# Optimization experiments

Measured on AMD Instinct MI355X. Metric: run time of the kernel, lower is better.

## Reference

```python
import jax, jax.numpy as jnp
import numpy as np

B, HG, WG = 2, 64, 64
N = HG * WG
C_IN, C_HID, HEADS, C_OUT = 512, 256, 4, 512
NEG_SLOPE = 0.2   # PyG GATv2Conv default negative_slope
LN_EPS = 1e-5


def _grid_edges(h, w):
    """8-neighborhood grid graph, edge_index[0]=source, edge_index[1]=target."""
    nodes = np.arange(h * w).reshape(h, w)
    srcs, dsts = [], []
    for dh in (-1, 0, 1):
        for dw in (-1, 0, 1):
            if dh == 0 and dw == 0:
                continue
            r0, r1 = max(0, -dh), h - max(0, dh)
            c0, c1 = max(0, -dw), w - max(0, dw)
            srcs.append(nodes[r0:r1, c0:c1].ravel())
            dsts.append(nodes[r0 + dh:r1 + dh, c0 + dw:c1 + dw].ravel())
    return np.stack([np.concatenate(srcs), np.concatenate(dsts)]).astype(np.int64)


def setup_inputs() -> dict:
    key = jax.random.key(0)
    ks = iter(jax.random.split(key, 32))

    def p(shape, scale=0.02):
        return jax.random.normal(next(ks), shape, dtype=jnp.float32) * scale

    return {
        "rgb_features": jax.random.normal(next(ks), (B, N, C_IN), dtype=jnp.float32),
        "x_features": jax.random.normal(next(ks), (B, N, C_IN), dtype=jnp.float32),
        "edge_index": jnp.asarray(_grid_edges(HG, WG)),
        # modality_fusion: Linear(2*C_IN, C_HID) + LayerNorm
        "fusion_w": p((C_HID, 2 * C_IN)), "fusion_b": jnp.zeros((C_HID,), jnp.float32),
        "fusion_g": jnp.ones((C_HID,), jnp.float32), "fusion_beta": jnp.zeros((C_HID,), jnp.float32),
        # GATSegmentation.in_proj + norm
        "inproj_w": p((C_HID, C_HID)), "inproj_b": jnp.zeros((C_HID,), jnp.float32),
        "norm_g": jnp.ones((C_HID,), jnp.float32), "norm_b": jnp.zeros((C_HID,), jnp.float32),
        # GATv2Conv layer 0: C_HID -> C_HID, heads=4, concat=True
        "l0_wl": p((HEADS * C_HID, C_HID)), "l0_bl": jnp.zeros((HEADS * C_HID,), jnp.float32),
        "l0_wr": p((HEADS * C_HID, C_HID)), "l0_br": jnp.zeros((HEADS * C_HID,), jnp.float32),
        "l0_att": p((HEADS, C_HID)), "l0_bias": jnp.zeros((HEADS * C_HID,), jnp.float32),
        # GATv2Conv layer 1 (final): 4*C_HID -> C_HID, heads=1, concat=False
        "l1_wl": p((C_HID, HEADS * C_HID)), "l1_bl": jnp.zeros((C_HID,), jnp.float32),
        "l1_wr": p((C_HID, HEADS * C_HID)), "l1_br": jnp.zeros((C_HID,), jnp.float32),
        "l1_att": p((1, C_HID)), "l1_bias": jnp.zeros((C_HID,), jnp.float32),
        # final_proj: 1x1 conv C_HID -> C_OUT
        "fp_w": p((C_OUT, C_HID)), "fp_b": jnp.zeros((C_OUT,), jnp.float32),
    }


def _ln(x, g, b):
    mu = x.mean(-1, keepdims=True)
    v = ((x - mu) ** 2).mean(-1, keepdims=True)
    return (x - mu) * jax.lax.rsqrt(v + LN_EPS) * g + b


def _gatv2(x, src, dst, wl, bl, wr, br, att, bias, concat):
    """PyG GATv2Conv (share_weights=False): gather, leaky_relu logit, segment softmax over
    target neighborhoods, scatter-add aggregation."""
    n = x.shape[0]
    heads, c = att.shape
    xl = (x @ wl.T + bl).reshape(n, heads, c)   # source-side transform (x_j)
    xr = (x @ wr.T + br).reshape(n, heads, c)   # target-side transform (x_i)
    e = jax.nn.leaky_relu(xl[src] + xr[dst], NEG_SLOPE)        # [E, H, C]
    logit = jnp.einsum('ehc,hc->eh', e, att)                   # [E, H]
    m = jax.ops.segment_max(logit, dst, num_segments=n)
    p = jnp.exp(logit - m[dst])
    z = jax.ops.segment_sum(p, dst, num_segments=n)
    alpha = p / z[dst]                                          # softmax per target node
    out = jax.ops.segment_sum(xl[src] * alpha[..., None], dst, num_segments=n)  # [N, H, C]
    out = out.reshape(n, heads * c) if concat else out.mean(axis=1)
    return out + bias


def reference(rgb_features, x_features, edge_index, fusion_w, fusion_b, fusion_g, fusion_beta,
              inproj_w, inproj_b, norm_g, norm_b,
              l0_wl, l0_bl, l0_wr, l0_br, l0_att, l0_bias,
              l1_wl, l1_bl, l1_wr, l1_br, l1_att, l1_bias,
              fp_w, fp_b):
    b, n, _ = rgb_features.shape
    loops = jnp.arange(n, dtype=edge_index.dtype)  # PyG add_self_loops=True
    src = jnp.concatenate([edge_index[0], loops])
    dst = jnp.concatenate([edge_index[1], loops])

    def single(rgb, xm):  # one graph in the batch (original loops over B in Python)
        comb = jnp.concatenate([rgb, xm], axis=-1)                     # [N, 2*C_IN]
        f = jax.nn.relu(_ln(comb @ fusion_w.T + fusion_b, fusion_g, fusion_beta))
        h = jax.nn.relu(_ln(f @ inproj_w.T + inproj_b, norm_g, norm_b))
        h = jax.nn.relu(_gatv2(h, src, dst, l0_wl, l0_bl, l0_wr, l0_br, l0_att, l0_bias, True))
        h = jax.nn.relu(_gatv2(h, src, dst, l1_wl, l1_bl, l1_wr, l1_br, l1_att, l1_bias, False))
        return h                                                        # [N, C_HID]

    nodes = jax.vmap(single)(rgb_features, x_features)                  # [B, N, C_HID]
    img = nodes.reshape(b, HG, WG, C_HID)
    return jnp.einsum('bhwc,oc->bohw', img, fp_w) + fp_b[None, :, None, None]
```

## Files before the change

### kernel.cpp

```cpp
#include <hip/hip_runtime.h>


#define NNODE 4096
#define LN_EPS 1e-5f
#define LOG2E 1.4426950408889634f

typedef _Float16 half8 __attribute__((ext_vector_type(8)));
typedef _Float16 half4 __attribute__((ext_vector_type(4)));
typedef _Float16 h2 __attribute__((ext_vector_type(2)));
typedef float f32x4 __attribute__((ext_vector_type(4)));

__device__ __forceinline__ float wave_reduce_sum(float v) {
    #pragma unroll
    for (int off = 32; off > 0; off >>= 1) v += __shfl_xor(v, off, 64);
    return v;
}

__device__ __forceinline__ void gload_lds16(const void* g, void* l) {
    __builtin_amdgcn_global_load_lds(
        (const __attribute__((address_space(1))) void*)g,
        (__attribute__((address_space(3))) void*)l, 16, 0, 0);
}

template<int N> __device__ __forceinline__ void waitcnt_vm() {
    if constexpr (N <= 0)      asm volatile("s_waitcnt vmcnt(0)" ::: "memory");
    else if constexpr (N == 2) asm volatile("s_waitcnt vmcnt(2)" ::: "memory");
    else if constexpr (N == 3) asm volatile("s_waitcnt vmcnt(3)" ::: "memory");
    else if constexpr (N == 4) asm volatile("s_waitcnt vmcnt(4)" ::: "memory");
    else                       asm volatile("s_waitcnt vmcnt(8)" ::: "memory");
}
__device__ __forceinline__ void lgkm0() {
    asm volatile("s_waitcnt lgkmcnt(0)" ::: "memory");
}
__device__ __forceinline__ void barrier_raw() {
    asm volatile("s_barrier" ::: "memory");
}

template<int IT, int JT, int OUTMODE>
__global__ __launch_bounds__(256) void gemm3_k(
    const _Float16* __restrict__ A, const _Float16* __restrict__ W,
    const float* __restrict__ bias_lo, const float* __restrict__ bias_hi,
    int nsplit, void* __restrict__ Cout, int K, int N)
{
    constexpr int BM = 32 * IT, BN = 32 * JT;
    constexpr int CA = (BM * 4) / 256;
    constexpr int CB = (BN * 4) / 256;
    constexpr int L = CA + CB;
    __shared__ _Float16 ldsA[3][BM * 32];
    __shared__ _Float16 ldsB[3][BN * 32];

    const int tid = threadIdx.x;
    const int m0 = blockIdx.y * BM, n0 = blockIdx.x * BN;
    const int lane = tid & 63, w = tid >> 6;
    const int fr = lane & 15, kq = lane >> 4;
    const int sq = (kq ^ (fr & 3)) * 8;
    const int wm = (w & 1) * (16 * IT), wn = (w >> 1) * (16 * JT);

    const _Float16* aP[CA]; int aC[CA];
    #pragma unroll
    for (int i = 0; i < CA; ++i) {
        const int c = i * 256 + tid, r = c >> 2, q = (c & 3) ^ (r & 3);
        aP[i] = A + (size_t)(m0 + r) * K + q * 8;
        aC[i] = c * 8;
    }
    const _Float16* bP[CB]; int bC[CB];
    #pragma unroll
    for (int i = 0; i < CB; ++i) {
        const int c = i * 256 + tid, r = c >> 2, q = (c & 3) ^ (r & 3);
        bP[i] = W + (size_t)(n0 + r) * K + q * 8;
        bC[i] = c * 8;
    }

    f32x4 acc[IT][JT] = {};
    const int NT = K >> 5;

    #pragma unroll
    for (int i = 0; i < CA; ++i) gload_lds16(aP[i], &ldsA[0][aC[i]]);
    #pragma unroll
    for (int i = 0; i < CB; ++i) gload_lds16(bP[i], &ldsB[0][bC[i]]);
    #pragma unroll
    for (int i = 0; i < CA; ++i) gload_lds16(aP[i] + 32, &ldsA[1][aC[i]]);
    #pragma unroll
    for (int i = 0; i < CB; ++i) gload_lds16(bP[i] + 32, &ldsB[1][bC[i]]);

    int bi = 0;
    for (int t = 0; t < NT; ++t) {
        if (t + 1 < NT) waitcnt_vm<L>(); else waitcnt_vm<0>();
        barrier_raw();
        if (t + 2 < NT) {
            int nb = bi + 2; if (nb >= 3) nb -= 3;
            const int k2 = (t + 2) << 5;
            #pragma unroll
            for (int i = 0; i < CA; ++i) gload_lds16(aP[i] + k2, &ldsA[nb][aC[i]]);
            #pragma unroll
            for (int i = 0; i < CB; ++i) gload_lds16(bP[i] + k2, &ldsB[nb][bC[i]]);
        }
        half8 af[IT], bf[JT];
        #pragma unroll
        for (int i = 0; i < IT; ++i)
            af[i] = *(const half8*)&ldsA[bi][(wm + i * 16 + fr) * 32 + sq];
        #pragma unroll
        for (int j = 0; j < JT; ++j)
            bf[j] = *(const half8*)&ldsB[bi][(wn + j * 16 + fr) * 32 + sq];
        #pragma unroll
        for (int i = 0; i < IT; ++i)
            #pragma unroll
            for (int j = 0; j < JT; ++j)
                acc[i][j] = __builtin_amdgcn_mfma_f32_16x16x32_f16(
                    bf[j], af[i], acc[i][j], 0, 0, 0);
        ++bi; if (bi == 3) bi = 0;
    }

    #pragma unroll
    for (int i = 0; i < IT; ++i) {
        const int m = m0 + wm + i * 16 + fr;
        #pragma unroll
        for (int j = 0; j < JT; ++j) {
            const int nb4 = n0 + wn + j * 16 + kq * 4;
            const float* bp = (nb4 < nsplit) ? bias_lo + nb4
                                             : bias_hi + (nb4 - nsplit);
            const float4 bv = *(const float4*)bp;
            half4 ov = {(_Float16)(acc[i][j][0] + bv.x),
                        (_Float16)(acc[i][j][1] + bv.y),
                        (_Float16)(acc[i][j][2] + bv.z),
                        (_Float16)(acc[i][j][3] + bv.w)};
            *(half4*)((_Float16*)Cout + (size_t)m * N + nb4) = ov;
        }
    }
}

struct ConvTab {
    const float* src[7];
    int startblk[8];
    int nelem[7];
    int dstoff[7];
    float scale[7];
};

__global__ __launch_bounds__(512) void fusion2b_k(
    const float* __restrict__ A0, const float* __restrict__ A1,
    const float* __restrict__ W1f, const float* __restrict__ b1,
    const float* __restrict__ g1, const float* __restrict__ be1,
    const float* __restrict__ W2f, const float* __restrict__ b2,
    const float* __restrict__ g2, const float* __restrict__ be2,
    _Float16* __restrict__ out, _Float16* __restrict__ wdst, ConvTab ct)
{
    if (blockIdx.x >= 256) {
        const int cid = blockIdx.x - 256;
        int s = 0;
        #pragma unroll
        for (int i = 1; i < 7; ++i) s += (cid >= ct.startblk[i]);
        const int e0 = (cid - ct.startblk[s]) * 2048 + threadIdx.x * 4;
        if (e0 < ct.nelem[s]) {
            const float4 v = *(const float4*)(ct.src[s] + e0);
            const float sc = ct.scale[s];
            half4 o = {(_Float16)(v.x * sc), (_Float16)(v.y * sc),
                       (_Float16)(v.z * sc), (_Float16)(v.w * sc)};
            *(half4*)(wdst + ct.dstoff[s] + e0) = o;
        }
        return;
    }

    __shared__ _Float16 lA[2][32 * 32];
    __shared__ _Float16 lB[2][256 * 32];
    __shared__ float lC[32 * 260];
    __shared__ _Float16 lH[8 * 1024];

    const int tid = threadIdx.x;
    const int m0 = blockIdx.x * 32;
    const int lane = tid & 63, w = tid >> 6;
    const int fr = lane & 15, kq = lane >> 4;
    const int sq = (kq ^ (fr & 3)) * 8;
    const int wr = (w & 1) * 16, wc = (w >> 1) * 64;
    const bool stager = (tid < 128);

    const int br_ = tid >> 3, bf_ = tid & 7;
    const int bq_ = bf_ >> 1, bo_ = bf_ & 1;
    float4 pb[4];

    const int ar = tid >> 2, aq = tid & 3;
    const int asw = (ar * 4 + (aq ^ (ar & 3))) * 8;
    float4 pa0, pa1;

    auto loadB = [&](const float* Wf, int ldw, int k0) {
        #pragma unroll
        for (int i = 0; i < 4; ++i)
            pb[i] = *(const float4*)(Wf + (size_t)(br_ + i * 64) * ldw + k0 + bf_ * 4);
    };
    auto writeB = [&](int buf) {
        #pragma unroll
        for (int i = 0; i < 4; ++i) {
            const int r = br_ + i * 64;
            half4 o = {(_Float16)pb[i].x, (_Float16)pb[i].y,
                       (_Float16)pb[i].z, (_Float16)pb[i].w};
            *(half4*)&lB[buf][(r * 4 + (bq_ ^ (r & 3))) * 8 + bo_ * 4] = o;
        }
    };
    auto loadA = [&](int k) {
        const int gk = k + aq * 8;
        const float* s = (gk < 512) ? A0 + (size_t)(m0 + ar) * 512 + gk
                                    : A1 + (size_t)(m0 + ar) * 512 + gk - 512;
        pa0 = *(const float4*)s;
        pa1 = *(const float4*)(s + 4);
    };
    auto writeA = [&](int buf) {
        half8 hv = {(_Float16)pa0.x, (_Float16)pa0.y, (_Float16)pa0.z, (_Float16)pa0.w,
                    (_Float16)pa1.x, (_Float16)pa1.y, (_Float16)pa1.z, (_Float16)pa1.w};
        *(half8*)&lA[buf][asw] = hv;
    };

    f32x4 acc1[4] = {};
    if (stager) { loadA(0); writeA(0); loadA(32); }
    loadB(W1f, 1024, 0); writeB(0); loadB(W1f, 1024, 32);
    lgkm0(); barrier_raw();
    for (int t = 0; t < 32; ++t) {
        if (t + 1 < 32) { writeB((t + 1) & 1); if (stager) writeA((t + 1) & 1); }
        lgkm0(); barrier_raw();
        if (t + 2 < 32) { loadB(W1f, 1024, (t + 2) * 32); if (stager) loadA((t + 2) * 32); }
        const half8 af = *(const half8*)&lA[t & 1][(wr + fr) * 32 + sq];
        half8 bfr[4];
        #pragma unroll
        for (int j = 0; j < 4; ++j)
            bfr[j] = *(const half8*)&lB[t & 1][(wc + j * 16 + fr) * 32 + sq];
        #pragma unroll
        for (int j = 0; j < 4; ++j)
            acc1[j] = __builtin_amdgcn_mfma_f32_16x16x32_f16(af, bfr[j], acc1[j], 0, 0, 0);
        lgkm0(); barrier_raw();
    }

    #pragma unroll
    for (int j = 0; j < 4; ++j) {
        const int col = wc + j * 16 + fr;
        const float bc = b1[col];
        #pragma unroll
        for (int r4 = 0; r4 < 4; ++r4)
            lC[(wr + kq * 4 + r4) * 260 + col] = acc1[j][r4] + bc;
    }
    __syncthreads();

    {
        const float4 gv = *(const float4*)(g1 + lane * 4);
        const float4 bv = *(const float4*)(be1 + lane * 4);
        const int t2i = lane >> 3, gq = (lane >> 1) & 3, qo = (lane & 1) * 4;
        #pragma unroll
        for (int rr = 0; rr < 4; ++rr) {
            const int row = w * 4 + rr;
            const float4 v = *(const float4*)&lC[row * 260 + lane * 4];
            float s  = v.x + v.y + v.z + v.w;
            float s2 = v.x * v.x + v.y * v.y + v.z * v.z + v.w * v.w;
            s = wave_reduce_sum(s);
            s2 = wave_reduce_sum(s2);
            const float mu  = s * (1.0f / 256.0f);
            const float var = s2 * (1.0f / 256.0f) - mu * mu;
            const float rs  = rsqrtf(var + LN_EPS);
            half4 o;
            o[0] = (_Float16)fmaxf((v.x - mu) * rs * gv.x + bv.x, 0.f);
            o[1] = (_Float16)fmaxf((v.y - mu) * rs * gv.y + bv.y, 0.f);
            o[2] = (_Float16)fmaxf((v.z - mu) * rs * gv.z + bv.z, 0.f);
            o[3] = (_Float16)fmaxf((v.w - mu) * rs * gv.w + bv.w, 0.f);
            const int qslot = gq ^ (row & 3);
            *(half4*)&lH[t2i * 1024 + (row * 4 + qslot) * 8 + qo] = o;
        }
    }
    __syncthreads();

    f32x4 acc2[4] = {};
    loadB(W2f, 256, 0); writeB(0); loadB(W2f, 256, 32);
    lgkm0(); barrier_raw();
    for (int t = 0; t < 8; ++t) {
        if (t + 1 < 8) writeB((t + 1) & 1);
        lgkm0(); barrier_raw();
        if (t + 2 < 8) loadB(W2f, 256, (t + 2) * 32);
        const half8 af = *(const half8*)
            &lH[t * 1024 + ((wr + fr) * 4 + (kq ^ (fr & 3))) * 8];
        half8 bfr[4];
        #pragma unroll
        for (int j = 0; j < 4; ++j)
            bfr[j] = *(const half8*)&lB[t & 1][(wc + j * 16 + fr) * 32 + sq];
        #pragma unroll
        for (int j = 0; j < 4; ++j)
            acc2[j] = __builtin_amdgcn_mfma_f32_16x16x32_f16(af, bfr[j], acc2[j], 0, 0, 0);
        lgkm0(); barrier_raw();
    }

    #pragma unroll
    for (int j = 0; j < 4; ++j) {
        const int col = wc + j * 16 + fr;
        const float bc = b2[col];
        #pragma unroll
        for (int r4 = 0; r4 < 4; ++r4)
            lC[(wr + kq * 4 + r4) * 260 + col] = acc2[j][r4] + bc;
    }
    __syncthreads();

    {
        const float4 gv = *(const float4*)(g2 + lane * 4);
        const float4 bv = *(const float4*)(be2 + lane * 4);
        #pragma unroll
        for (int rr = 0; rr < 4; ++rr) {
            const int row = w * 4 + rr;
            const float4 v = *(const float4*)&lC[row * 260 + lane * 4];
            float s  = v.x + v.y + v.z + v.w;
            float s2 = v.x * v.x + v.y * v.y + v.z * v.z + v.w * v.w;
            s = wave_reduce_sum(s);
            s2 = wave_reduce_sum(s2);
            const float mu  = s * (1.0f / 256.0f);
            const float var = s2 * (1.0f / 256.0f) - mu * mu;
            const float rs  = rsqrtf(var + LN_EPS);
            half4 o;
            o[0] = (_Float16)fmaxf((v.x - mu) * rs * gv.x + bv.x, 0.f);
            o[1] = (_Float16)fmaxf((v.y - mu) * rs * gv.y + bv.y, 0.f);
            o[2] = (_Float16)fmaxf((v.z - mu) * rs * gv.z + bv.z, 0.f);
            o[3] = (_Float16)fmaxf((v.w - mu) * rs * gv.w + bv.w, 0.f);
            *(half4*)(out + (size_t)(m0 + row) * 256 + lane * 4) = o;
        }
    }
}

template<int HEADS, int K, int LD, int XROFF, int OUTMODE>
__global__ __launch_bounds__(512) void gatgemm_k(
    const _Float16* __restrict__ xlr, const _Float16* __restrict__ att16,
    const float* __restrict__ gbias, const _Float16* __restrict__ W,
    const float* __restrict__ bias_lo, const float* __restrict__ bias_hi,
    int nsplit, void* __restrict__ Cout)
{
    constexpr int PAD = K + 8;
    constexpr int NT = K / 32;
    __shared__ _Float16 lA[32 * PAD];
    __shared__ _Float16 lB[2][512 * 32];

    const int tid = threadIdx.x;
    const int m0 = blockIdx.x * 32;
    const int lane = tid & 63, w = tid >> 6;
    const int g = lane >> 4, li = lane & 15;

    const _Float16* bP[4]; int bC[4];
    #pragma unroll
    for (int i = 0; i < 4; ++i) {
        const int c = i * 512 + tid, r = c >> 2, q = (c & 3) ^ (r & 3);
        bP[i] = W + (size_t)r * K + q * 8;
        bC[i] = c * 8;
    }
    #pragma unroll
    for (int i = 0; i < 4; ++i) gload_lds16(bP[i], &lB[0][bC[i]]);
    #pragma unroll
    for (int i = 0; i < 4; ++i) gload_lds16(bP[i] + 32, &lB[1][bC[i]]);

    const int rounds = (HEADS == 4) ? 4 : 1;
    for (int rr = 0; rr < rounds; ++rr) {
        const int row = (HEADS == 4) ? (w * 4 + rr) : (w * 4 + g);
        const int gi = m0 + row;
        const int node = gi & (NNODE - 1);
        const int base = gi - node;
        const int h = (HEADS == 4) ? g : 0;
        const int nr = node >> 6, nc = node & 63;
        const int co = h * 256 + li * 16;

        int sidx[9]; float msk[9];
        {
            const int drs[8] = {-1,-1,-1, 0, 0, 1, 1, 1};
            const int dcs[8] = {-1, 0, 1,-1, 1,-1, 0, 1};
            #pragma unroll
            for (int j = 0; j < 8; ++j) {
                const int rj = nr + drs[j], cj = nc + dcs[j];
                const bool v = ((unsigned)rj < 64u) & ((unsigned)cj < 64u);
                sidx[j] = v ? (rj * 64 + cj) : node;
                msk[j] = v ? 0.f : -1e30f;
            }
            sidx[8] = node; msk[8] = 0.f;
        }
        const _Float16* xp = xlr + (size_t)base * LD + co;
        const half8 xr0 = *(const half8*)(xlr + (size_t)gi * LD + XROFF + co);
        const half8 xr1 = *(const half8*)(xlr + (size_t)gi * LD + XROFF + co + 8);
        const half8 at0 = *(const half8*)(att16 + h * 256 + li * 16);
        const half8 at1 = *(const half8*)(att16 + h * 256 + li * 16 + 8);
        const h2 hz = {(_Float16)0.f, (_Float16)0.f};
        const h2 c02 = {(_Float16)0.2f, (_Float16)0.2f};

        float lg[9];
        #pragma unroll
        for (int j = 0; j < 9; ++j) {
            const half8 x0 = *(const half8*)(xp + (size_t)sidx[j] * LD);
            const half8 x1 = *(const half8*)(xp + (size_t)sidx[j] * LD + 8);
            h2 p = hz;
            #pragma unroll
            for (int k = 0; k < 4; ++k) {
                h2 e = ((const h2*)&x0)[k] + ((const h2*)&xr0)[k];
                h2 tt = __builtin_elementwise_fma(
                    __builtin_elementwise_min(e, hz), c02,
                    __builtin_elementwise_max(e, hz));
                p = __builtin_elementwise_fma(tt, ((const h2*)&at0)[k], p);
            }
            #pragma unroll
            for (int k = 0; k < 4; ++k) {
                h2 e = ((const h2*)&x1)[k] + ((const h2*)&xr1)[k];
                h2 tt = __builtin_elementwise_fma(
                    __builtin_elementwise_min(e, hz), c02,
                    __builtin_elementwise_max(e, hz));
                p = __builtin_elementwise_fma(tt, ((const h2*)&at1)[k], p);
            }
            float pl = (float)p[0] + (float)p[1];
            pl += __shfl_xor(pl, 1, 64);
            pl += __shfl_xor(pl, 2, 64);
            pl += __shfl_xor(pl, 4, 64);
            pl += __shfl_xor(pl, 8, 64);
            lg[j] = pl + msk[j];
        }
        float m = lg[0];
        #pragma unroll
        for (int j = 1; j < 9; ++j) m = fmaxf(m, lg[j]);
        float pj[9], z = 0.f;
        #pragma unroll
        for (int j = 0; j < 9; ++j) { pj[j] = __builtin_amdgcn_exp2f(lg[j] - m); z += pj[j]; }
        const float inv = __builtin_amdgcn_rcpf(z);

        float acc[16];
        #pragma unroll
        for (int k = 0; k < 16; ++k) acc[k] = 0.f;
        #pragma unroll
        for (int j = 0; j < 9; ++j) {
            const half8 x0 = *(const half8*)(xp + (size_t)sidx[j] * LD);
            const half8 x1 = *(const half8*)(xp + (size_t)sidx[j] * LD + 8);
            const float wj = pj[j];
            #pragma unroll
            for (int k = 0; k < 8; ++k) acc[k]     += wj * (float)x0[k];
            #pragma unroll
            for (int k = 0; k < 8; ++k) acc[8 + k] += wj * (float)x1[k];
        }
        float bv[16];
        #pragma unroll
        for (int q = 0; q < 4; ++q) {
            const float4 b4 = *(const float4*)(gbias + h * 256 + li * 16 + q * 4);
            bv[q * 4 + 0] = b4.x; bv[q * 4 + 1] = b4.y;
            bv[q * 4 + 2] = b4.z; bv[q * 4 + 3] = b4.w;
        }
        half8 o0, o1;
        #pragma unroll
        for (int k = 0; k < 8; ++k) o0[k] = (_Float16)fmaxf(acc[k] * inv + bv[k], 0.f);
        #pragma unroll
        for (int k = 0; k < 8; ++k) o1[k] = (_Float16)fmaxf(acc[8 + k] * inv + bv[8 + k], 0.f);
        *(half8*)&lA[row * PAD + co] = o0;
        *(half8*)&lA[row * PAD + co + 8] = o1;
    }
    __syncthreads();

    const int fr = lane & 15, kq = lane >> 4;
    const int sq = (kq ^ (fr & 3)) * 8;
    const int wc = w * 64;
    f32x4 acc[2][4] = {};

    for (int t = 0; t < NT; ++t) {
        if (t + 1 < NT) waitcnt_vm<4>(); else waitcnt_vm<0>();
        barrier_raw();
        half8 af[2]; half8 bfr[4];
        #pragma unroll
        for (int i = 0; i < 2; ++i)
            af[i] = *(const half8*)&lA[(i * 16 + fr) * PAD + t * 32 + kq * 8];
        #pragma unroll
        for (int j = 0; j < 4; ++j)
            bfr[j] = *(const half8*)&lB[t & 1][(wc + j * 16 + fr) * 32 + sq];
        lgkm0(); barrier_raw();
        if (t + 2 < NT) {
            #pragma unroll
            for (int i = 0; i < 4; ++i)
                gload_lds16(bP[i] + (t + 2) * 32, &lB[t & 1][bC[i]]);
        }
        #pragma unroll
        for (int i = 0; i < 2; ++i)
            #pragma unroll
            for (int j = 0; j < 4; ++j) {
                if (OUTMODE == 1)
                    acc[i][j] = __builtin_amdgcn_mfma_f32_16x16x32_f16(
                        bfr[j], af[i], acc[i][j], 0, 0, 0);
                else
                    acc[i][j] = __builtin_amdgcn_mfma_f32_16x16x32_f16(
                        af[i], bfr[j], acc[i][j], 0, 0, 0);
            }
    }

    if (OUTMODE == 1) {
        #pragma unroll
        for (int i = 0; i < 2; ++i) {
            const int m = m0 + i * 16 + fr;
            #pragma unroll
            for (int j = 0; j < 4; ++j) {
                const int nb4 = wc + j * 16 + kq * 4;
                const float* bp = (nb4 < nsplit) ? bias_lo + nb4
                                                 : bias_hi + (nb4 - nsplit);
                const float4 bvv = *(const float4*)bp;
                half4 ov = {(_Float16)(acc[i][j][0] + bvv.x),
                            (_Float16)(acc[i][j][1] + bvv.y),
                            (_Float16)(acc[i][j][2] + bvv.z),
                            (_Float16)(acc[i][j][3] + bvv.w)};
                *(half4*)((_Float16*)Cout + (size_t)m * 512 + nb4) = ov;
            }
        }
    } else {
        #pragma unroll
        for (int j = 0; j < 4; ++j) {
            const int col = wc + j * 16 + fr;
            const float bc = bias_lo[col];
            #pragma unroll
            for (int i = 0; i < 2; ++i) {
                const int mrun = m0 + i * 16 + kq * 4;
                const int b = mrun >> 12, node = mrun & 4095;
                float4 ov = {acc[i][j][0] + bc, acc[i][j][1] + bc,
                             acc[i][j][2] + bc, acc[i][j][3] + bc};
                *(float4*)((float*)Cout + ((size_t)(b * 512 + col)) * 4096 + node) = ov;
            }
        }
    }
}

extern "C" void kernel_launch(void* const* d_in, const int* in_sizes, int n_in,
                              void* d_out, int out_size, void* d_ws, size_t ws_size,
                              hipStream_t stream)
{
    const float* rgb       = (const float*)d_in[0];
    const float* xm        = (const float*)d_in[1];
    const float* fusion_w  = (const float*)d_in[3];
    const float* fusion_b  = (const float*)d_in[4];
    const float* fusion_g  = (const float*)d_in[5];
    const float* fusion_be = (const float*)d_in[6];
    const float* inproj_w  = (const float*)d_in[7];
    const float* inproj_b  = (const float*)d_in[8];
    const float* norm_g    = (const float*)d_in[9];
    const float* norm_b    = (const float*)d_in[10];
    const float* l0_wl     = (const float*)d_in[11];
    const float* l0_bl     = (const float*)d_in[12];
    const float* l0_wr     = (const float*)d_in[13];
    const float* l0_br     = (const float*)d_in[14];
    const float* l0_att    = (const float*)d_in[15];
    const float* l0_bias   = (const float*)d_in[16];
    const float* l1_wl     = (const float*)d_in[17];
    const float* l1_bl     = (const float*)d_in[18];
    const float* l1_wr     = (const float*)d_in[19];
    const float* l1_br     = (const float*)d_in[20];
    const float* l1_att    = (const float*)d_in[21];
    const float* l1_bias   = (const float*)d_in[22];
    const float* fp_w      = (const float*)d_in[23];
    const float* fp_b      = (const float*)d_in[24];

    char* ws = (char*)d_ws;
    _Float16* Wf16 = (_Float16*)ws;
    _Float16* H1   = (_Float16*)(ws + 4194304);
    _Float16* XLR0 = (_Float16*)(ws + 8388608);
    _Float16* XLR1 = (_Float16*)(ws + 41943040);

    _Float16* w_l0   = Wf16 + 327680;
    _Float16* w_l1   = Wf16 + 851968;
    _Float16* w_fp   = Wf16 + 1376256;
    _Float16* att0_h = Wf16 + 1507328;
    _Float16* att1_h = Wf16 + 1508352;

    ConvTab ct;
    const float* srcs[7] = {l0_wl, l0_wr, l1_wl, l1_wr, fp_w, l0_att, l1_att};
    const int nel[7]  = {262144, 262144, 262144, 262144, 131072, 1024, 256};
    const int doff[7] = {327680, 589824, 851968, 1114112, 1376256, 1507328, 1508352};
    const int sblk[8] = {0, 128, 256, 384, 512, 576, 577, 578};
    for (int i = 0; i < 7; ++i) {
        ct.src[i] = srcs[i]; ct.nelem[i] = nel[i]; ct.dstoff[i] = doff[i];
        ct.scale[i] = (i >= 5) ? LOG2E : 1.0f;
    }
    for (int i = 0; i < 8; ++i) ct.startblk[i] = sblk[i];

    fusion2b_k<<<834, 512, 0, stream>>>(
        rgb, xm, fusion_w, fusion_b, fusion_g, fusion_be,
        inproj_w, inproj_b, norm_g, norm_b, H1, Wf16, ct);

    gemm3_k<4, 4, 1><<<dim3(16, 64), 256, 0, stream>>>(
        H1, w_l0, l0_bl, l0_br, 1024, XLR0, 256, 2048);

    gatgemm_k<4, 1024, 2048, 1024, 1><<<256, 512, 0, stream>>>(
        XLR0, att0_h, l0_bias, w_l1, l1_bl, l1_br, 256, XLR1);

    gatgemm_k<1, 256, 512, 256, 2><<<256, 512, 0, stream>>>(
        XLR1, att1_h, l1_bias, w_fp, fp_b, fp_b, 512, d_out);
}
```

Measured before the change: 127.3 us.

## Split fused GAT+GEMM kernels into standalone attention and GEMM launches

Replaces the fused attention-plus-GEMM kernel, which ran only 256 blocks of 512 threads with heavy LDS use, with a separate wave-per-node attention kernel that writes an fp16 intermediate, followed by the general pipelined GEMM kernel. The GEMM kernel gains a transposed-output mode so it can write the final NCHW float output. The aim is better occupancy and a more efficient GEMM pipeline. The cost is two extra launches and a round trip of the attention outputs through global memory. The attention kernel also preloads all nine neighbour vectors into registers instead of loading them twice.

```diff
diff --git a/kernel.cpp b/kernel.cpp
--- a/kernel.cpp
+++ b/kernel.cpp
@@ -105,26 +105,47 @@
         #pragma unroll
         for (int i = 0; i < IT; ++i)
             #pragma unroll
-            for (int j = 0; j < JT; ++j)
-                acc[i][j] = __builtin_amdgcn_mfma_f32_16x16x32_f16(
-                    bf[j], af[i], acc[i][j], 0, 0, 0);
+            for (int j = 0; j < JT; ++j) {
+                if (OUTMODE == 1)
+                    acc[i][j] = __builtin_amdgcn_mfma_f32_16x16x32_f16(
+                        bf[j], af[i], acc[i][j], 0, 0, 0);
+                else
+                    acc[i][j] = __builtin_amdgcn_mfma_f32_16x16x32_f16(
+                        af[i], bf[j], acc[i][j], 0, 0, 0);
+            }
         ++bi; if (bi == 3) bi = 0;
     }
 
-    #pragma unroll
-    for (int i = 0; i < IT; ++i) {
-        const int m = m0 + wm + i * 16 + fr;
+    if (OUTMODE == 1) {
+        #pragma unroll
+        for (int i = 0; i < IT; ++i) {
+            const int m = m0 + wm + i * 16 + fr;
+            #pragma unroll
+            for (int j = 0; j < JT; ++j) {
+                const int nb4 = n0 + wn + j * 16 + kq * 4;
+                const float* bp = (nb4 < nsplit) ? bias_lo + nb4
+                                                 : bias_hi + (nb4 - nsplit);
+                const float4 bv = *(const float4*)bp;
+                half4 ov = {(_Float16)(acc[i][j][0] + bv.x),
+                            (_Float16)(acc[i][j][1] + bv.y),
+                            (_Float16)(acc[i][j][2] + bv.z),
+                            (_Float16)(acc[i][j][3] + bv.w)};
+                *(half4*)((_Float16*)Cout + (size_t)m * N + nb4) = ov;
+            }
+        }
+    } else {
         #pragma unroll
         for (int j = 0; j < JT; ++j) {
-            const int nb4 = n0 + wn + j * 16 + kq * 4;
-            const float* bp = (nb4 < nsplit) ? bias_lo + nb4
-                                             : bias_hi + (nb4 - nsplit);
-            const float4 bv = *(const float4*)bp;
-            half4 ov = {(_Float16)(acc[i][j][0] + bv.x),
-                        (_Float16)(acc[i][j][1] + bv.y),
-                        (_Float16)(acc[i][j][2] + bv.z),
-                        (_Float16)(acc[i][j][3] + bv.w)};
-            *(half4*)((_Float16*)Cout + (size_t)m * N + nb4) = ov;
+            const int col = n0 + wn + j * 16 + fr;
+            const float bc = (col < nsplit) ? bias_lo[col] : bias_hi[col - nsplit];
+            #pragma unroll
+            for (int i = 0; i < IT; ++i) {
+                const int mrun = m0 + wm + i * 16 + kq * 4;
+                const int b = mrun >> 12, node = mrun & 4095;
+                float4 ov = {acc[i][j][0] + bc, acc[i][j][1] + bc,
+                             acc[i][j][2] + bc, acc[i][j][3] + bc};
+                *(float4*)((float*)Cout + ((size_t)(b * N + col)) * 4096 + node) = ov;
+            }
         }
     }
 }
@@ -317,199 +338,111 @@
     }
 }
 
-template<int HEADS, int K, int LD, int XROFF, int OUTMODE>
-__global__ __launch_bounds__(512) void gatgemm_k(
+template<int HEADS, int LD, int XROFF, int OC>
+__global__ __launch_bounds__(256) void gat4_k(
     const _Float16* __restrict__ xlr, const _Float16* __restrict__ att16,
-    const float* __restrict__ gbias, const _Float16* __restrict__ W,
-    const float* __restrict__ bias_lo, const float* __restrict__ bias_hi,
-    int nsplit, void* __restrict__ Cout)
+    const float* __restrict__ bias, _Float16* __restrict__ out)
 {
-    constexpr int PAD = K + 8;
-    constexpr int NT = K / 32;
-    __shared__ _Float16 lA[32 * PAD];
-    __shared__ _Float16 lB[2][512 * 32];
-
-    const int tid = threadIdx.x;
-    const int m0 = blockIdx.x * 32;
-    const int lane = tid & 63, w = tid >> 6;
+    const int tid = threadIdx.x, wv = tid >> 6, lane = tid & 63;
     const int g = lane >> 4, li = lane & 15;
-
-    const _Float16* bP[4]; int bC[4];
-    #pragma unroll
-    for (int i = 0; i < 4; ++i) {
-        const int c = i * 512 + tid, r = c >> 2, q = (c & 3) ^ (r & 3);
-        bP[i] = W + (size_t)r * K + q * 8;
-        bC[i] = c * 8;
-    }
-    #pragma unroll
-    for (int i = 0; i < 4; ++i) gload_lds16(bP[i], &lB[0][bC[i]]);
-    #pragma unroll
-    for (int i = 0; i < 4; ++i) gload_lds16(bP[i] + 32, &lB[1][bC[i]]);
-
-    const int rounds = (HEADS == 4) ? 4 : 1;
-    for (int rr = 0; rr < rounds; ++rr) {
-        const int row = (HEADS == 4) ? (w * 4 + rr) : (w * 4 + g);
-        const int gi = m0 + row;
-        const int node = gi & (NNODE - 1);
-        const int base = gi - node;
-        const int h = (HEADS == 4) ? g : 0;
-        const int nr = node >> 6, nc = node & 63;
-        const int co = h * 256 + li * 16;
-
-        int sidx[9]; float msk[9];
-        {
-            const int drs[8] = {-1,-1,-1, 0, 0, 1, 1, 1};
-            const int dcs[8] = {-1, 0, 1,-1, 1,-1, 0, 1};
-            #pragma unroll
-            for (int j = 0; j < 8; ++j) {
-                const int rj = nr + drs[j], cj = nc + dcs[j];
-                const bool v = ((unsigned)rj < 64u) & ((unsigned)cj < 64u);
-                sidx[j] = v ? (rj * 64 + cj) : node;
-                msk[j] = v ? 0.f : -1e30f;
-            }
-            sidx[8] = node; msk[8] = 0.f;
-        }
-        const _Float16* xp = xlr + (size_t)base * LD + co;
-        const half8 xr0 = *(const half8*)(xlr + (size_t)gi * LD + XROFF + co);
-        const half8 xr1 = *(const half8*)(xlr + (size_t)gi * LD + XROFF + co + 8);
-        const half8 at0 = *(const half8*)(att16 + h * 256 + li * 16);
-        const half8 at1 = *(const half8*)(att16 + h * 256 + li * 16 + 8);
-        const h2 hz = {(_Float16)0.f, (_Float16)0.f};
-        const h2 c02 = {(_Float16)0.2f, (_Float16)0.2f};
-
-        float lg[9];
-        #pragma unroll
-        for (int j = 0; j < 9; ++j) {
-            const half8 x0 = *(const half8*)(xp + (size_t)sidx[j] * LD);
-            const half8 x1 = *(const half8*)(xp + (size_t)sidx[j] * LD + 8);
-            h2 p = hz;
-            #pragma unroll
-            for (int k = 0; k < 4; ++k) {
-                h2 e = ((const h2*)&x0)[k] + ((const h2*)&xr0)[k];
-                h2 tt = __builtin_elementwise_fma(
-                    __builtin_elementwise_min(e, hz), c02,
-                    __builtin_elementwise_max(e, hz));
-                p = __builtin_elementwise_fma(tt, ((const h2*)&at0)[k], p);
-            }
-            #pragma unroll
-            for (int k = 0; k < 4; ++k) {
-                h2 e = ((const h2*)&x1)[k] + ((const h2*)&xr1)[k];
-                h2 tt = __builtin_elementwise_fma(
-                    __builtin_elementwise_min(e, hz), c02,
-                    __builtin_elementwise_max(e, hz));
-                p = __builtin_elementwise_fma(tt, ((const h2*)&at1)[k], p);
-            }
-            float pl = (float)p[0] + (float)p[1];
-            pl += __shfl_xor(pl, 1, 64);
-            pl += __shfl_xor(pl, 2, 64);
-            pl += __shfl_xor(pl, 4, 64);
-            pl += __shfl_xor(pl, 8, 64);
-            lg[j] = pl + msk[j];
-        }
-        float m = lg[0];
-        #pragma unroll
-        for (int j = 1; j < 9; ++j) m = fmaxf(m, lg[j]);
-        float pj[9], z = 0.f;
-        #pragma unroll
-        for (int j = 0; j < 9; ++j) { pj[j] = __builtin_amdgcn_exp2f(lg[j] - m); z += pj[j]; }
-        const float inv = __builtin_amdgcn_rcpf(z);
-
-        float acc[16];
-        #pragma unroll
-        for (int k = 0; k < 16; ++k) acc[k] = 0.f;
-        #pragma unroll
-        for (int j = 0; j < 9; ++j) {
-            const half8 x0 = *(const half8*)(xp + (size_t)sidx[j] * LD);
-            const half8 x1 = *(const half8*)(xp + (size_t)sidx[j] * LD + 8);
-            const float wj = pj[j];
-            #pragma unroll
-            for (int k = 0; k < 8; ++k) acc[k]     += wj * (float)x0[k];
-            #pragma unroll
-            for (int k = 0; k < 8; ++k) acc[8 + k] += wj * (float)x1[k];
-        }
-        float bv[16];
-        #pragma unroll
-        for (int q = 0; q < 4; ++q) {
-            const float4 b4 = *(const float4*)(gbias + h * 256 + li * 16 + q * 4);
-            bv[q * 4 + 0] = b4.x; bv[q * 4 + 1] = b4.y;
-            bv[q * 4 + 2] = b4.z; bv[q * 4 + 3] = b4.w;
-        }
-        half8 o0, o1;
-        #pragma unroll
-        for (int k = 0; k < 8; ++k) o0[k] = (_Float16)fmaxf(acc[k] * inv + bv[k], 0.f);
-        #pragma unroll
-        for (int k = 0; k < 8; ++k) o1[k] = (_Float16)fmaxf(acc[8 + k] * inv + bv[8 + k], 0.f);
-        *(half8*)&lA[row * PAD + co] = o0;
-        *(half8*)&lA[row * PAD + co + 8] = o1;
-    }
-    __syncthreads();
-
-    const int fr = lane & 15, kq = lane >> 4;
-    const int sq = (kq ^ (fr & 3)) * 8;
-    const int wc = w * 64;
-    f32x4 acc[2][4] = {};
-
-    for (int t = 0; t < NT; ++t) {
-        if (t + 1 < NT) waitcnt_vm<4>(); else waitcnt_vm<0>();
-        barrier_raw();
-        half8 af[2]; half8 bfr[4];
-        #pragma unroll
-        for (int i = 0; i < 2; ++i)
-            af[i] = *(const half8*)&lA[(i * 16 + fr) * PAD + t * 32 + kq * 8];
-        #pragma unroll
-        for (int j = 0; j < 4; ++j)
-            bfr[j] = *(const half8*)&lB[t & 1][(wc + j * 16 + fr) * 32 + sq];
-        lgkm0(); barrier_raw();
-        if (t + 2 < NT) {
-            #pragma unroll
-            for (int i = 0; i < 4; ++i)
-                gload_lds16(bP[i] + (t + 2) * 32, &lB[t & 1][bC[i]]);
-        }
-        #pragma unroll
-        for (int i = 0; i < 2; ++i)
-            #pragma unroll
-            for (int j = 0; j < 4; ++j) {
-                if (OUTMODE == 1)
-                    acc[i][j] = __builtin_amdgcn_mfma_f32_16x16x32_f16(
-                        bfr[j], af[i], acc[i][j], 0, 0, 0);
-                else
-                    acc[i][j] = __builtin_amdgcn_mfma_f32_16x16x32_f16(
-                        af[i], bfr[j], acc[i][j], 0, 0, 0);
-            }
-    }
-
-    if (OUTMODE == 1) {
-        #pragma unroll
-        for (int i = 0; i < 2; ++i) {
-            const int m = m0 + i * 16 + fr;
-            #pragma unroll
-            for (int j = 0; j < 4; ++j) {
-                const int nb4 = wc + j * 16 + kq * 4;
-                const float* bp = (nb4 < nsplit) ? bias_lo + nb4
-                                                 : bias_hi + (nb4 - nsplit);
-                const float4 bvv = *(const float4*)bp;
-                half4 ov = {(_Float16)(acc[i][j][0] + bvv.x),
-                            (_Float16)(acc[i][j][1] + bvv.y),
-                            (_Float16)(acc[i][j][2] + bvv.z),
-                            (_Float16)(acc[i][j][3] + bvv.w)};
-                *(half4*)((_Float16*)Cout + (size_t)m * 512 + nb4) = ov;
-            }
-        }
-    } else {
-        #pragma unroll
-        for (int j = 0; j < 4; ++j) {
-            const int col = wc + j * 16 + fr;
-            const float bc = bias_lo[col];
-            #pragma unroll
-            for (int i = 0; i < 2; ++i) {
-                const int mrun = m0 + i * 16 + kq * 4;
-                const int b = mrun >> 12, node = mrun & 4095;
-                float4 ov = {acc[i][j][0] + bc, acc[i][j][1] + bc,
-                             acc[i][j][2] + bc, acc[i][j][3] + bc};
-                *(float4*)((float*)Cout + ((size_t)(b * 512 + col)) * 4096 + node) = ov;
-            }
-        }
-    }
+    const int wid = blockIdx.x * 4 + wv;
+    const int gi = (HEADS == 4) ? wid : wid * 4 + g;
+    const int h  = (HEADS == 4) ? g : 0;
+    const int node = gi & (NNODE - 1);
+    const int base = gi - node;
+    const int nr = node >> 6, nc = node & 63;
+    const int co = h * 256 + li * 16;
+
+    int sidx[9]; float msk[9];
+    {
+        const int drs[8] = {-1,-1,-1, 0, 0, 1, 1, 1};
+        const int dcs[8] = {-1, 0, 1,-1, 1,-1, 0, 1};
+        #pragma unroll
+        for (int j = 0; j < 8; ++j) {
+            const int rj = nr + drs[j], cj = nc + dcs[j];
+            const bool v = ((unsigned)rj < 64u) & ((unsigned)cj < 64u);
+            sidx[j] = v ? (rj * 64 + cj) : node;
+            msk[j] = v ? 0.f : -1e30f;
+        }
+        sidx[8] = node; msk[8] = 0.f;
+    }
+
+    const _Float16* xp = xlr + (size_t)base * LD + co;
+
+    half8 x0[9], x1[9];
+    #pragma unroll
+    for (int j = 0; j < 9; ++j) {
+        x0[j] = *(const half8*)(xp + (size_t)sidx[j] * LD);
+        x1[j] = *(const half8*)(xp + (size_t)sidx[j] * LD + 8);
+    }
+    const half8 xr0 = *(const half8*)(xlr + (size_t)gi * LD + XROFF + co);
+    const half8 xr1 = *(const half8*)(xlr + (size_t)gi * LD + XROFF + co + 8);
+    const half8 at0 = *(const half8*)(att16 + h * 256 + li * 16);
+    const half8 at1 = *(const half8*)(att16 + h * 256 + li * 16 + 8);
+    const h2 hz = {(_Float16)0.f, (_Float16)0.f};
+    const h2 c02 = {(_Float16)0.2f, (_Float16)0.2f};
+
+    float lg[9];
+    #pragma unroll
+    for (int j = 0; j < 9; ++j) {
+        h2 p = hz;
+        #pragma unroll
+        for (int k = 0; k < 4; ++k) {
+            h2 e = ((const h2*)&x0[j])[k] + ((const h2*)&xr0)[k];
+            h2 tt = __builtin_elementwise_fma(
+                __builtin_elementwise_min(e, hz), c02,
+                __builtin_elementwise_max(e, hz));
+            p = __builtin_elementwise_fma(tt, ((const h2*)&at0)[k], p);
+        }
+        #pragma unroll
+        for (int k = 0; k < 4; ++k) {
+            h2 e = ((const h2*)&x1[j])[k] + ((const h2*)&xr1)[k];
+            h2 tt = __builtin_elementwise_fma(
+                __builtin_elementwise_min(e, hz), c02,
+                __builtin_elementwise_max(e, hz));
+            p = __builtin_elementwise_fma(tt, ((const h2*)&at1)[k], p);
+        }
+        float pl = (float)p[0] + (float)p[1];
+        pl += __shfl_xor(pl, 1, 64);
+        pl += __shfl_xor(pl, 2, 64);
+        pl += __shfl_xor(pl, 4, 64);
+        pl += __shfl_xor(pl, 8, 64);
+        lg[j] = pl + msk[j];
+    }
+
+    float m = lg[0];
+    #pragma unroll
+    for (int j = 1; j < 9; ++j) m = fmaxf(m, lg[j]);
+    float pj[9], z = 0.f;
+    #pragma unroll
+    for (int j = 0; j < 9; ++j) { pj[j] = __builtin_amdgcn_exp2f(lg[j] - m); z += pj[j]; }
+    const float inv = __builtin_amdgcn_rcpf(z);
+
+    float acc[16];
+    #pragma unroll
+    for (int k = 0; k < 16; ++k) acc[k] = 0.f;
+    #pragma unroll
+    for (int j = 0; j < 9; ++j) {
+        const float wj = pj[j];
+        #pragma unroll
+        for (int k = 0; k < 8; ++k) acc[k]     += wj * (float)x0[j][k];
+        #pragma unroll
+        for (int k = 0; k < 8; ++k) acc[8 + k] += wj * (float)x1[j][k];
+    }
+    float bv[16];
+    #pragma unroll
+    for (int q = 0; q < 4; ++q) {
+        const float4 b4 = *(const float4*)(bias + h * 256 + li * 16 + q * 4);
+        bv[q * 4 + 0] = b4.x; bv[q * 4 + 1] = b4.y;
+        bv[q * 4 + 2] = b4.z; bv[q * 4 + 3] = b4.w;
+    }
+    half8 o0, o1;
+    #pragma unroll
+    for (int k = 0; k < 8; ++k) o0[k] = (_Float16)fmaxf(acc[k] * inv + bv[k], 0.f);
+    #pragma unroll
+    for (int k = 0; k < 8; ++k) o1[k] = (_Float16)fmaxf(acc[8 + k] * inv + bv[8 + k], 0.f);
+    *(half8*)(out + (size_t)gi * OC + co) = o0;
+    *(half8*)(out + (size_t)gi * OC + co + 8) = o1;
 }
 
 extern "C" void kernel_launch(void* const* d_in, const int* in_sizes, int n_in,
@@ -545,7 +478,9 @@
     _Float16* Wf16 = (_Float16*)ws;
     _Float16* H1   = (_Float16*)(ws + 4194304);
     _Float16* XLR0 = (_Float16*)(ws + 8388608);
-    _Float16* XLR1 = (_Float16*)(ws + 41943040);
+    _Float16* GO0  = (_Float16*)(ws + 41943040);
+    _Float16* XLR1 = (_Float16*)(ws + 58720256);
+    _Float16* GO1  = (_Float16*)(ws + 67108864);
 
     _Float16* w_l0   = Wf16 + 327680;
     _Float16* w_l1   = Wf16 + 851968;
@@ -571,9 +506,15 @@
     gemm3_k<4, 4, 1><<<dim3(16, 64), 256, 0, stream>>>(
         H1, w_l0, l0_bl, l0_br, 1024, XLR0, 256, 2048);
 
-    gatgemm_k<4, 1024, 2048, 1024, 1><<<256, 512, 0, stream>>>(
-        XLR0, att0_h, l0_bias, w_l1, l1_bl, l1_br, 256, XLR1);
-
-    gatgemm_k<1, 256, 512, 256, 2><<<256, 512, 0, stream>>>(
-        XLR1, att1_h, l1_bias, w_fp, fp_b, fp_b, 512, d_out);
-}
+    gat4_k<4, 2048, 1024, 1024><<<2048, 256, 0, stream>>>(
+        XLR0, att0_h, l0_bias, GO0);
+
+    gemm3_k<2, 4, 1><<<dim3(4, 128), 256, 0, stream>>>(
+        GO0, w_l1, l1_bl, l1_br, 256, XLR1, 1024, 512);
+
+    gat4_k<1, 512, 256, 256><<<512, 256, 0, stream>>>(
+        XLR1, att1_h, l1_bias, GO1);
+
+    gemm3_k<2, 4, 2><<<dim3(4, 128), 256, 0, stream>>>(
+        GO1, w_fp, fp_b, fp_b, 512, d_out, 256, 512);
+}
```

Result: faster. 121.2 us (median of 2 runs) (-4.7%).
